# Performance work log

Hardware: AMD Instinct MI355X
Metric: run time of the kernel (lower is better)

The kernel has to match this reference:

```python
import jax, jax.numpy as jnp
import numpy as np

D, H, DH = 768, 12, 64
W = 256            # one-sided window (attention_window=512 total)
EPS = 1e-6
NEG = -1e9


def layer_norm(x, g, b):
    m = jnp.mean(x, axis=-1, keepdims=True)
    v = jnp.mean((x - m) ** 2, axis=-1, keepdims=True)
    return g * (x - m) * jax.lax.rsqrt(v + EPS) + b


def _blocks3(t, nb):
    # t: [B,H,nb,W,dh] -> keys/values of 3 neighboring blocks [B,H,nb,3W,dh]
    tp = jnp.pad(t, ((0, 0), (0, 0), (1, 1), (0, 0), (0, 0)))
    return jnp.concatenate([tp[:, :, :nb], tp[:, :, 1:nb + 1], tp[:, :, 2:nb + 2]], axis=3)


def sliding_window_attention(x, kpm, Wq, bq, Wk, bk, Wv, bv, Wo, bo):
    B, S, _ = x.shape
    nb = S // W
    def proj(Wm, bm):
        return (x @ Wm + bm).reshape(B, S, H, DH).transpose(0, 2, 1, 3).reshape(B, H, nb, W, DH)
    q = proj(Wq, bq) * (1.0 / np.sqrt(DH))
    k = proj(Wk, bk)
    v = proj(Wv, bv)
    k3 = _blocks3(k, nb)
    v3 = _blocks3(v, nb)
    # scores over local band: [B,H,nb,W,3W]
    s = jnp.einsum('bhnqd,bhnkd->bhnqk', q, k3)
    qi = jnp.arange(W)[:, None]
    kj = jnp.arange(3 * W)[None, :]
    band = jnp.abs(kj - W - qi) <= W                     # [W,3W]
    kg = (jnp.arange(nb)[:, None, None] - 1) * W + kj[None]  # global key idx [nb,1,3W]
    inrange = (kg >= 0) & (kg < S)
    # key padding mask gathered into block layout: [B,nb,3W]
    kpm_b = jnp.pad(kpm.reshape(B, nb, W), ((0, 0), (1, 1), (0, 0)), constant_values=True)
    kpm3 = jnp.concatenate([kpm_b[:, :nb], kpm_b[:, 1:nb + 1], kpm_b[:, 2:nb + 2]], axis=2)
    m = band[None, None, None] & inrange[None, None] & (~kpm3)[:, None, :, None, :]
    s = jnp.where(m, s, NEG)
    p = jax.nn.softmax(s, axis=-1)
    o = jnp.einsum('bhnqk,bhnkd->bhnqd', p, v3)
    o = o.reshape(B, H, S, DH).transpose(0, 2, 1, 3).reshape(B, S, D)
    return o @ Wo + bo


def setup_inputs() -> dict:
    key = jax.random.key(0)
    ks = jax.random.split(key, 12)
    B, S, DF = 2, 4096, 3072
    sc = 1.0 / np.sqrt(D)
    return {
        'x': jax.random.normal(ks[0], (B, S, D), jnp.float32),
        'mask': jnp.zeros((B, S), bool),
        'id': 0,
        'Wq': jax.random.normal(ks[1], (D, D), jnp.float32) * sc,
        'bq': jnp.zeros((D,), jnp.float32),
        'Wk': jax.random.normal(ks[2], (D, D), jnp.float32) * sc,
        'bk': jnp.zeros((D,), jnp.float32),
        'Wv': jax.random.normal(ks[3], (D, D), jnp.float32) * sc,
        'bv': jnp.zeros((D,), jnp.float32),
        'Wo': jax.random.normal(ks[4], (D, D), jnp.float32) * sc,
        'bo': jnp.zeros((D,), jnp.float32),
        'ln1_g': jnp.ones((D,), jnp.float32),
        'ln1_b': jnp.zeros((D,), jnp.float32),
        'W1': jax.random.normal(ks[5], (D, DF), jnp.float32) * sc,
        'b1': jnp.zeros((DF,), jnp.float32),
        'W2': jax.random.normal(ks[6], (DF, D), jnp.float32) * (1.0 / np.sqrt(DF)),
        'b2': jnp.zeros((D,), jnp.float32),
        'ln2_g': jnp.ones((D,), jnp.float32),
        'ln2_b': jnp.zeros((D,), jnp.float32),
    }


def reference(x, mask, id, Wq, bq, Wk, bk, Wv, bv, Wo, bo, ln1_g, ln1_b, W1, b1, W2, b2, ln2_g, ln2_b):
    # Sublayer 1: pre-norm residual around sliding-window self-attention
    h = layer_norm(x, ln1_g, ln1_b)
    x = x + sliding_window_attention(h, mask, Wq, bq, Wk, bk, Wv, bv, Wo, bo)
    # Sublayer 2: pre-norm residual around positionwise FFN
    h = layer_norm(x, ln2_g, ln2_b)
    x = x + (jax.nn.relu(h @ W1 + b1) @ W2 + b2)
    return x
```

## Files before the change

kernel.cpp:

```cpp
#include <hip/hip_runtime.h>
#include <hip/hip_bf16.h>
#include <cstddef>

typedef __attribute__((ext_vector_type(8))) short short8;
typedef __attribute__((ext_vector_type(4))) float f32x4;
typedef __attribute__((ext_vector_type(4))) unsigned short us4;

typedef __attribute__((address_space(1))) void as1_void;
typedef __attribute__((address_space(3))) void as3_void;

__device__ __forceinline__ void gload16(const void* g, void* lds) {
  __builtin_amdgcn_global_load_lds((as1_void*)(void*)g, (as3_void*)lds, 16, 0, 0);
}

__device__ inline unsigned short f2bf(float f) {
  union { float f; unsigned int u; } v; v.f = f;
  return (unsigned short)((v.u + 0x7FFFu + ((v.u >> 16) & 1u)) >> 16);
}

__device__ __forceinline__ float exp2v(float x) {
  float r; asm("v_exp_f32 %0, %1" : "=v"(r) : "v"(x)); return r;
}
__device__ __forceinline__ unsigned cvtpk(float a, float b) {
  unsigned r; asm("v_cvt_pk_bf16_f32 %0, %1, %2" : "=v"(r) : "v"(a), "v"(b)); return r;
}

__global__ __launch_bounds__(256) void ln_kernel(const float* __restrict__ x,
    const float* __restrict__ g, const float* __restrict__ b,
    unsigned short* __restrict__ out)
{
  int row = blockIdx.x, t = threadIdx.x;
  const float* xr = x + (size_t)row * 768;
  float v0 = xr[t], v1 = xr[t + 256], v2 = xr[t + 512];
  float s = v0 + v1 + v2;
  #pragma unroll
  for (int o = 32; o > 0; o >>= 1) s += __shfl_xor(s, o);
  __shared__ float r1[4], r2[4];
  if ((t & 63) == 0) r1[t >> 6] = s;
  __syncthreads();
  float mean = (r1[0] + r1[1] + r1[2] + r1[3]) * (1.0f / 768.0f);
  float d0 = v0 - mean, d1 = v1 - mean, d2 = v2 - mean;
  float q = d0 * d0 + d1 * d1 + d2 * d2;
  #pragma unroll
  for (int o = 32; o > 0; o >>= 1) q += __shfl_xor(q, o);
  if ((t & 63) == 0) r2[t >> 6] = q;
  __syncthreads();
  float var = (r2[0] + r2[1] + r2[2] + r2[3]) * (1.0f / 768.0f);
  float rs = rsqrtf(var + 1e-6f);
  unsigned short* orow = out + (size_t)row * 768;
  orow[t]       = f2bf(g[t]       * d0 * rs + b[t]);
  orow[t + 256] = f2bf(g[t + 256] * d1 * rs + b[t + 256]);
  orow[t + 512] = f2bf(g[t + 512] * d2 * rs + b[t + 512]);
}

__global__ __launch_bounds__(256) void prep_kernel(
    const float* __restrict__ Wq, const float* __restrict__ Wk,
    const float* __restrict__ Wv, const float* __restrict__ Wo,
    const float* __restrict__ W1, const float* __restrict__ W2,
    const float* __restrict__ bq, const float* __restrict__ bk,
    const float* __restrict__ bv,
    unsigned short* __restrict__ WTqkv, unsigned short* __restrict__ WTo,
    unsigned short* __restrict__ W1T, unsigned short* __restrict__ W2T,
    float* __restrict__ bqkv,
    const float* __restrict__ x, const float* __restrict__ ln1g,
    const float* __restrict__ ln1b, unsigned short* __restrict__ hbuf)
{
  int bid = blockIdx.x;
  int t = threadIdx.x;
  if (bid >= 6921) {
    int row = bid - 6921;
    const float* xr = x + (size_t)row * 768;
    float v0 = xr[t], v1 = xr[t + 256], v2 = xr[t + 512];
    float s = v0 + v1 + v2;
    #pragma unroll
    for (int o = 32; o > 0; o >>= 1) s += __shfl_xor(s, o);
    __shared__ float r1[4], r2[4];
    if ((t & 63) == 0) r1[t >> 6] = s;
    __syncthreads();
    float mean = (r1[0] + r1[1] + r1[2] + r1[3]) * (1.0f / 768.0f);
    float d0 = v0 - mean, d1 = v1 - mean, d2 = v2 - mean;
    float q = d0 * d0 + d1 * d1 + d2 * d2;
    #pragma unroll
    for (int o = 32; o > 0; o >>= 1) q += __shfl_xor(q, o);
    if ((t & 63) == 0) r2[t >> 6] = q;
    __syncthreads();
    float var = (r2[0] + r2[1] + r2[2] + r2[3]) * (1.0f / 768.0f);
    float rs = rsqrtf(var + 1e-6f);
    unsigned short* orow = hbuf + (size_t)row * 768;
    orow[t]       = f2bf(ln1g[t]       * d0 * rs + ln1b[t]);
    orow[t + 256] = f2bf(ln1g[t + 256] * d1 * rs + ln1b[t + 256]);
    orow[t + 512] = f2bf(ln1g[t + 512] * d2 * rs + ln1b[t + 512]);
    return;
  }
  if (bid >= 6912) {
    int i = (bid - 6912) * 256 + t;
    bqkv[i] = (i < 768) ? bq[i] : ((i < 1536) ? bk[i - 768] : bv[i - 1536]);
    return;
  }
  const float* W; unsigned short* WT; int K, N, lb;
  if (bid < 576)       { W = Wq; WT = WTqkv;                        K = 768;  N = 768;  lb = bid; }
  else if (bid < 1152) { W = Wk; WT = WTqkv + (size_t)768 * 768;    K = 768;  N = 768;  lb = bid - 576; }
  else if (bid < 1728) { W = Wv; WT = WTqkv + (size_t)1536 * 768;   K = 768;  N = 768;  lb = bid - 1152; }
  else if (bid < 2304) { W = Wo; WT = WTo;                          K = 768;  N = 768;  lb = bid - 1728; }
  else if (bid < 4608) { W = W1; WT = W1T;                          K = 768;  N = 3072; lb = bid - 2304; }
  else                 { W = W2; WT = W2T;                          K = 3072; N = 768;  lb = bid - 4608; }
  int ntN = N >> 5;
  int k0 = (lb / ntN) * 32, n0 = (lb % ntN) * 32;
  __shared__ float tile[32][33];
  int tx = t & 31, ty = t >> 5;
  #pragma unroll
  for (int i = 0; i < 32; i += 8)
    tile[ty + i][tx] = W[(size_t)(k0 + ty + i) * N + n0 + tx];
  __syncthreads();
  #pragma unroll
  for (int i = 0; i < 32; i += 8)
    WT[(size_t)(n0 + ty + i) * K + k0 + tx] = f2bf(tile[tx][ty + i]);
}

enum { EPI_QKV = 0, EPI_RELU = 1, EPI_RESID = 2 };

template<int EPI>
__global__ __launch_bounds__(256, 2) void gemmW_kernel(
    const unsigned short* __restrict__ A, const unsigned short* __restrict__ BT,
    const float* __restrict__ bias, const float* __restrict__ resid,
    void* __restrict__ outp, int M, int N, int K, int ntn)
{
  __shared__ char lds[2][40960];
  int tid = threadIdx.x;
  int nwg = gridDim.x;
  int bid = ((int)blockIdx.x & 7) * (nwg >> 3) + ((int)blockIdx.x >> 3);
  int mt = bid / ntn, nt = bid % ntn;
  int m0 = mt * 64, n0 = nt * 256;
  int w = tid >> 6, l = tid & 63;
  int fr = l & 15, fq = l >> 4;
  int rb = tid >> 3;
  int sw8 = ((tid & 7) ^ (rb & 7)) * 8;
  const unsigned short* As = A  + (size_t)(m0 + rb) * K + sw8;
  const unsigned short* Bs = BT + (size_t)(n0 + rb) * K + sw8;

  auto stage = [&](int buf, int kt) {
    char* d = &lds[buf][0] + tid * 16;
    #pragma unroll
    for (int c = 0; c < 2; c++)
      gload16(As + (size_t)(c * 32) * K + kt * 64, d + c * 4096);
    #pragma unroll
    for (int c = 0; c < 8; c++)
      gload16(Bs + (size_t)(c * 32) * K + kt * 64, d + 8192 + c * 4096);
  };

  f32x4 acc[4][4] = {};
  stage(0, 0);
  asm volatile("s_waitcnt vmcnt(0)" ::: "memory");
  __syncthreads();

  int NT = K >> 6;
  for (int t = 0; t < NT; ++t) {
    int R = t & 1;
    if (t + 1 < NT) stage(R ^ 1, t + 1);
    #pragma unroll
    for (int h = 0; h < 2; h++) {
      short8 af[4], bf[4];
      const char* base = &lds[R][0];
      int colb = (h * 64 + fq * 16) ^ ((fr & 7) << 4);
      #pragma unroll
      for (int i = 0; i < 4; i++)
        af[i] = *(const short8*)(base + (i * 16 + fr) * 128 + colb);
      #pragma unroll
      for (int j = 0; j < 4; j++)
        bf[j] = *(const short8*)(base + 8192 + (w * 64 + j * 16 + fr) * 128 + colb);
      __builtin_amdgcn_s_setprio(1);
      #pragma unroll
      for (int i = 0; i < 4; i++)
        #pragma unroll
        for (int j = 0; j < 4; j++)
          acc[i][j] = __builtin_amdgcn_mfma_f32_16x16x32_bf16(af[i], bf[j], acc[i][j], 0, 0, 0);
      __builtin_amdgcn_s_setprio(0);
    }
    asm volatile("s_waitcnt vmcnt(0)" ::: "memory");
    __syncthreads();
  }

  #pragma unroll
  for (int nj = 0; nj < 4; nj++) {
    int col = n0 + w * 64 + nj * 16 + fr;
    float bs = bias[col];
    if (EPI == EPI_QKV) {
      int which = (col >= 1536) ? 2 : ((col >= 768) ? 1 : 0);
      int c2 = col - which * 768;
      int hh = c2 >> 6, dh = c2 & 63;
      if (which == 2) {
        unsigned short* dstv = reinterpret_cast<unsigned short*>(outp) + (size_t)2 * 8192 * 768;
        #pragma unroll
        for (int i = 0; i < 4; i++) {
          int row0 = m0 + i * 16 + fq * 4;
          int bb = row0 >> 12, sl = row0 & 4095;
          us4 pv;
          #pragma unroll
          for (int r = 0; r < 4; r++) pv[r] = f2bf(acc[i][nj][r] + bs);
          *reinterpret_cast<us4*>(&dstv[((size_t)(bb * 12 + hh) * 64 + dh) * 4096 + sl]) = pv;
        }
      } else {
        unsigned short* dst = reinterpret_cast<unsigned short*>(outp) + (size_t)which * 8192 * 768;
        #pragma unroll
        for (int i = 0; i < 4; i++) {
          #pragma unroll
          for (int r = 0; r < 4; r++) {
            int row = m0 + i * 16 + fq * 4 + r;
            float c = acc[i][nj][r] + bs;
            if (which == 0) c *= 0.18033688011112042f;
            int bb = row >> 12, sl = row & 4095;
            dst[(((size_t)(bb * 12 + hh)) * 4096 + sl) * 64 + dh] = f2bf(c);
          }
        }
      }
    } else if (EPI == EPI_RELU) {
      #pragma unroll
      for (int i = 0; i < 4; i++)
        #pragma unroll
        for (int r = 0; r < 4; r++) {
          int row = m0 + i * 16 + fq * 4 + r;
          float c = fmaxf(acc[i][nj][r] + bs, 0.0f);
          reinterpret_cast<unsigned short*>(outp)[(size_t)row * N + col] = f2bf(c);
        }
    } else {
      #pragma unroll
      for (int i = 0; i < 4; i++)
        #pragma unroll
        for (int r = 0; r < 4; r++) {
          int row = m0 + i * 16 + fq * 4 + r;
          float c = acc[i][nj][r] + bs + resid[(size_t)row * N + col];
          reinterpret_cast<float*>(outp)[(size_t)row * N + col] = c;
        }
    }
  }
}

__global__ __launch_bounds__(256) void attn_fused_kernel(
    const unsigned short* __restrict__ qg, const unsigned short* __restrict__ kg,
    const unsigned short* __restrict__ vtg, const unsigned char* __restrict__ kpm,
    unsigned short* __restrict__ attn_out)
{
  __shared__ unsigned short lds_k[3][64 * 64];
  __shared__ unsigned short lds_vt[3][64 * 64];
  __shared__ unsigned short lds_p[4][32 * 64];
  int bid0 = blockIdx.x;
  int bid = (bid0 & 7) * 96 + (bid0 >> 3);
  int qblk = bid & 31, h = (bid >> 5) % 12, b = bid / 384;
  int bh = b * 12 + h;
  int q0 = qblk * 128;
  int tid = threadIdx.x, w = tid >> 6, l = tid & 63;
  int fr = l & 15, fq = l >> 4;
  int qw0 = q0 + w * 32;
  int swzb = (((l & 7) ^ (l >> 3)) << 4);
  const char* qbase  = (const char*)(qg  + (size_t)bh * 4096 * 64);
  const char* kbase  = (const char*)(kg  + (size_t)bh * 4096 * 64);
  const char* vtbase = (const char*)(vtg + (size_t)bh * 64 * 4096);
  const unsigned char* kpmb = kpm + (size_t)b * 4096;

  #pragma unroll
  for (int s = 0; s < 4; s++) {
    int row = w * 32 + s * 8 + (l >> 3);
    gload16(qbase + (size_t)(q0 + row) * 128 + swzb, (char*)lds_p[w] + s * 1024);
  }

  auto stageKVc = [&](int c, int buf) {
    int g0 = q0 - 256 + c * 64;
    g0 = (g0 < 0) ? 0 : ((g0 > 4032) ? 4032 : g0);
    #pragma unroll
    for (int s = 0; s < 2; s++) {
      int row = w * 16 + s * 8 + (l >> 3);
      gload16(kbase + (size_t)(g0 + row) * 128 + swzb,
              (char*)lds_k[buf] + (w * 2 + s) * 1024);
      gload16(vtbase + ((size_t)row * 4096 + g0) * 2 + swzb,
              (char*)lds_vt[buf] + (w * 2 + s) * 1024);
    }
  };

  stageKVc(0, 0);
  stageKVc(1, 1);
  asm volatile("s_waitcnt vmcnt(8)" ::: "memory");

  short8 qf[2][2];
  #pragma unroll
  for (int i = 0; i < 2; i++)
    #pragma unroll
    for (int ks = 0; ks < 2; ks++)
      qf[i][ks] = *(const short8*)((const char*)lds_p[w] + (i * 16 + fr) * 128 +
                    ((ks * 64 + fq * 16) ^ ((fr & 7) << 4)));

  f32x4 acc_o[2][4] = {};
  float m_st[2] = {-3.0e38f, -3.0e38f};
  float l_st[2] = {0.0f, 0.0f};

  for (int c = 0; c < 10; c++) {
    if (c < 9) { asm volatile("s_waitcnt vmcnt(4)" ::: "memory"); }
    else       { asm volatile("s_waitcnt vmcnt(0)" ::: "memory"); }
    __builtin_amdgcn_s_barrier();
    if (c < 8) stageKVc(c + 2, (c + 2) % 3);
    int g0 = q0 - 256 + c * 64;
    bool valid = (g0 >= 0) && (g0 < 4096);
    if (valid) {
      int buf = c % 3;
      unsigned int km[4];
      #pragma unroll
      for (int j = 0; j < 4; j++)
        km[j] = *(const unsigned int*)(kpmb + g0 + 16 * j + 4 * fq);
      bool anyk = __any((km[0] | km[1] | km[2] | km[3]) != 0);
      int rel = g0 - qw0;
      bool edge = anyk || (rel < -225) || (rel > 193);
      short8 kf[4][2];
      #pragma unroll
      for (int j = 0; j < 4; j++)
        #pragma unroll
        for (int ks = 0; ks < 2; ks++)
          kf[j][ks] = *(const short8*)((const char*)lds_k[buf] + (j * 16 + fr) * 128 +
                        ((ks * 64 + fq * 16) ^ ((fr & 7) << 4)));
      f32x4 accs[4][2] = {};
      #pragma unroll
      for (int j = 0; j < 4; j++)
        #pragma unroll
        for (int i = 0; i < 2; i++)
          #pragma unroll
          for (int ks = 0; ks < 2; ks++)
            accs[j][i] = __builtin_amdgcn_mfma_f32_16x16x32_bf16(kf[j][ks], qf[i][ks], accs[j][i], 0, 0, 0);
      #pragma unroll
      for (int i = 0; i < 2; i++) {
        float sv[4][4];
        #pragma unroll
        for (int j = 0; j < 4; j++)
          #pragma unroll
          for (int r = 0; r < 4; r++)
            sv[j][r] = accs[j][i][r];
        if (edge) {
          int base = rel + 4 * fq - fr - 16 * i;
          #pragma unroll
          for (int j = 0; j < 4; j++)
            #pragma unroll
            for (int r = 0; r < 4; r++) {
              int d = base + 16 * j + r;
              bool ok = (d >= -256) && (d <= 256) && (((km[j] >> (8 * r)) & 255u) == 0u);
              if (!ok) sv[j][r] = -1.0e9f;
            }
        }
        float mv = sv[0][0];
        #pragma unroll
        for (int j = 0; j < 4; j++)
          #pragma unroll
          for (int r = 0; r < 4; r++) mv = fmaxf(mv, sv[j][r]);
        mv = fmaxf(mv, __shfl_xor(mv, 16));
        mv = fmaxf(mv, __shfl_xor(mv, 32));
        float mo = m_st[i];
        if (!__all(mv - mo <= 8.0f)) {
          float mn = fmaxf(mo, mv);
          float scl = exp2v(mo - mn);
          l_st[i] *= scl;
          m_st[i] = mn;
          #pragma unroll
          for (int r = 0; r < 4; r++) {
            float so = __shfl(scl, (l & 48) | ((l >> 2) & 12) | r);
            #pragma unroll
            for (int jd = 0; jd < 4; jd++) acc_o[i][jd][r] *= so;
          }
        }
        float mn = m_st[i];
        float rs = 0.0f;
        char* prow = (char*)lds_p[w] + (i * 16 + fr) * 128;
        #pragma unroll
        for (int j = 0; j < 4; j++) {
          float p0 = exp2v(sv[j][0] - mn), p1 = exp2v(sv[j][1] - mn);
          float p2 = exp2v(sv[j][2] - mn), p3 = exp2v(sv[j][3] - mn);
          rs += (p0 + p1) + (p2 + p3);
          uint2 u; u.x = cvtpk(p0, p1); u.y = cvtpk(p2, p3);
          *(uint2*)(prow + ((32 * j + 8 * fq) ^ ((fr & 7) << 4))) = u;
        }
        rs += __shfl_xor(rs, 16);
        rs += __shfl_xor(rs, 32);
        l_st[i] += rs;
      }
      short8 pf[2][2];
      #pragma unroll
      for (int i = 0; i < 2; i++)
        #pragma unroll
        for (int ks = 0; ks < 2; ks++)
          pf[i][ks] = *(const short8*)((const char*)lds_p[w] + (i * 16 + fr) * 128 +
                        ((ks * 64 + fq * 16) ^ ((fr & 7) << 4)));
      short8 vf[4][2];
      #pragma unroll
      for (int jd = 0; jd < 4; jd++)
        #pragma unroll
        for (int ks = 0; ks < 2; ks++)
          vf[jd][ks] = *(const short8*)((const char*)lds_vt[buf] + (jd * 16 + fr) * 128 +
                        ((ks * 64 + fq * 16) ^ ((fr & 7) << 4)));
      #pragma unroll
      for (int i = 0; i < 2; i++)
        #pragma unroll
        for (int jd = 0; jd < 4; jd++)
          #pragma unroll
          for (int ks = 0; ks < 2; ks++)
            acc_o[i][jd] = __builtin_amdgcn_mfma_f32_16x16x32_bf16(pf[i][ks], vf[jd][ks], acc_o[i][jd], 0, 0, 0);
    }
  }
  #pragma unroll
  for (int i = 0; i < 2; i++) {
    #pragma unroll
    for (int r = 0; r < 4; r++) {
      float lv = __shfl(l_st[i], (l & 48) | ((l >> 2) & 12) | r);
      float inv = 1.0f / lv;
      int qrow = qw0 + i * 16 + fq * 4 + r;
      size_t orow = ((size_t)b * 4096 + qrow) * 768 + h * 64;
      #pragma unroll
      for (int jd = 0; jd < 4; jd++)
        attn_out[orow + jd * 16 + fr] = f2bf(acc_o[i][jd][r] * inv);
    }
  }
}

extern "C" void kernel_launch(void* const* d_in, const int* in_sizes, int n_in,
                              void* d_out, int out_size, void* d_ws, size_t ws_size,
                              hipStream_t stream) {
  const float* x            = (const float*)d_in[0];
  const unsigned char* mask = (const unsigned char*)d_in[1];
  const float* Wq  = (const float*)d_in[3];
  const float* bq  = (const float*)d_in[4];
  const float* Wk  = (const float*)d_in[5];
  const float* bk  = (const float*)d_in[6];
  const float* Wv  = (const float*)d_in[7];
  const float* bv  = (const float*)d_in[8];
  const float* Wo  = (const float*)d_in[9];
  const float* bo  = (const float*)d_in[10];
  const float* ln1g = (const float*)d_in[11];
  const float* ln1b = (const float*)d_in[12];
  const float* W1  = (const float*)d_in[13];
  const float* b1  = (const float*)d_in[14];
  const float* W2  = (const float*)d_in[15];
  const float* b2  = (const float*)d_in[16];
  const float* ln2g = (const float*)d_in[17];
  const float* ln2b = (const float*)d_in[18];
  float* out = (float*)d_out;

  char* ws = (char*)d_ws;
  size_t off = 0;
  auto alloc = [&](size_t bytes) -> void* {
    void* p = ws + off;
    off += (bytes + 255) & ~(size_t)255;
    return p;
  };
  unsigned short* WTqkv = (unsigned short*)alloc((size_t)2304 * 768 * 2);
  unsigned short* WTo   = (unsigned short*)alloc((size_t)768 * 768 * 2);
  unsigned short* W1T   = (unsigned short*)alloc((size_t)3072 * 768 * 2);
  unsigned short* W2T   = (unsigned short*)alloc((size_t)768 * 3072 * 2);
  float*          bqkv  = (float*)alloc(2304 * 4);
  unsigned short* hbuf  = (unsigned short*)alloc((size_t)8192 * 768 * 2);
  unsigned short* qkv   = (unsigned short*)alloc((size_t)3 * 8192 * 768 * 2);
  unsigned short* attn  = (unsigned short*)alloc((size_t)8192 * 768 * 2);
  float* x1             = (float*)alloc((size_t)8192 * 768 * 4);
  unsigned short* h2    = (unsigned short*)alloc((size_t)8192 * 768 * 2);
  unsigned short* a1    = (unsigned short*)alloc((size_t)8192 * 3072 * 2);

  prep_kernel<<<15113, 256, 0, stream>>>(Wq, Wk, Wv, Wo, W1, W2, bq, bk, bv,
                                         WTqkv, WTo, W1T, W2T, bqkv,
                                         x, ln1g, ln1b, hbuf);

  gemmW_kernel<EPI_QKV><<<1152, 256, 0, stream>>>(hbuf, WTqkv, bqkv, nullptr, qkv, 8192, 2304, 768, 9);

  attn_fused_kernel<<<768, 256, 0, stream>>>(qkv, qkv + (size_t)8192 * 768,
                                             qkv + (size_t)2 * 8192 * 768, mask, attn);

  gemmW_kernel<EPI_RESID><<<384, 256, 0, stream>>>(attn, WTo, bo, x, x1, 8192, 768, 768, 3);
  ln_kernel<<<8192, 256, 0, stream>>>(x1, ln2g, ln2b, h2);
  gemmW_kernel<EPI_RELU><<<1536, 256, 0, stream>>>(h2, W1T, b1, nullptr, a1, 8192, 3072, 768, 12);
  gemmW_kernel<EPI_RESID><<<384, 256, 0, stream>>>(a1, W2T, b2, x1, out, 8192, 768, 3072, 3);
}
```

Before: 244.1 us.

## Switch GEMMs to square 128x128 tiles with single-buffered LDS

Replaces the 64x256 double-buffered GEMM tile with a 128x128 tile over a 2x2 wave grid, using one LDS buffer per operand and no prefetch of the next K step. Square tiles cut total global traffic per output and halve LDS use, which may allow more resident workgroups per CU. In exchange, loads for each K step are no longer overlapped with the MFMA work of the previous one, so every iteration waits on memory with two barriers.

New measurement: 250.4 us. 1.03x slower.

```diff
diff --git a/kernel.cpp b/kernel.cpp
--- a/kernel.cpp
+++ b/kernel.cpp
@@ -120,54 +120,51 @@
 enum { EPI_QKV = 0, EPI_RELU = 1, EPI_RESID = 2 };
 
 template<int EPI>
-__global__ __launch_bounds__(256, 2) void gemmW_kernel(
+__global__ __launch_bounds__(256) void gemmS_kernel(
     const unsigned short* __restrict__ A, const unsigned short* __restrict__ BT,
     const float* __restrict__ bias, const float* __restrict__ resid,
     void* __restrict__ outp, int M, int N, int K, int ntn)
 {
-  __shared__ char lds[2][40960];
+  __shared__ char lds_a[16384];
+  __shared__ char lds_b[16384];
   int tid = threadIdx.x;
   int nwg = gridDim.x;
   int bid = ((int)blockIdx.x & 7) * (nwg >> 3) + ((int)blockIdx.x >> 3);
   int mt = bid / ntn, nt = bid % ntn;
-  int m0 = mt * 64, n0 = nt * 256;
+  int m0 = mt * 128, n0 = nt * 128;
   int w = tid >> 6, l = tid & 63;
+  int wr = w >> 1, wc = w & 1;
   int fr = l & 15, fq = l >> 4;
   int rb = tid >> 3;
   int sw8 = ((tid & 7) ^ (rb & 7)) * 8;
   const unsigned short* As = A  + (size_t)(m0 + rb) * K + sw8;
   const unsigned short* Bs = BT + (size_t)(n0 + rb) * K + sw8;
 
-  auto stage = [&](int buf, int kt) {
-    char* d = &lds[buf][0] + tid * 16;
-    #pragma unroll
-    for (int c = 0; c < 2; c++)
-      gload16(As + (size_t)(c * 32) * K + kt * 64, d + c * 4096);
-    #pragma unroll
-    for (int c = 0; c < 8; c++)
-      gload16(Bs + (size_t)(c * 32) * K + kt * 64, d + 8192 + c * 4096);
-  };
-
   f32x4 acc[4][4] = {};
-  stage(0, 0);
-  asm volatile("s_waitcnt vmcnt(0)" ::: "memory");
-  __syncthreads();
-
   int NT = K >> 6;
   for (int t = 0; t < NT; ++t) {
-    int R = t & 1;
-    if (t + 1 < NT) stage(R ^ 1, t + 1);
+    {
+      char* dA = lds_a + tid * 16;
+      char* dB = lds_b + tid * 16;
+      int ko = t * 64;
+      #pragma unroll
+      for (int c = 0; c < 4; c++) {
+        gload16(As + (size_t)(c * 32) * K + ko, dA + c * 4096);
+        gload16(Bs + (size_t)(c * 32) * K + ko, dB + c * 4096);
+      }
+    }
+    asm volatile("s_waitcnt vmcnt(0)" ::: "memory");
+    __syncthreads();
     #pragma unroll
     for (int h = 0; h < 2; h++) {
       short8 af[4], bf[4];
-      const char* base = &lds[R][0];
       int colb = (h * 64 + fq * 16) ^ ((fr & 7) << 4);
       #pragma unroll
       for (int i = 0; i < 4; i++)
-        af[i] = *(const short8*)(base + (i * 16 + fr) * 128 + colb);
+        af[i] = *(const short8*)(lds_a + (wr * 64 + i * 16 + fr) * 128 + colb);
       #pragma unroll
       for (int j = 0; j < 4; j++)
-        bf[j] = *(const short8*)(base + 8192 + (w * 64 + j * 16 + fr) * 128 + colb);
+        bf[j] = *(const short8*)(lds_b + (wc * 64 + j * 16 + fr) * 128 + colb);
       __builtin_amdgcn_s_setprio(1);
       #pragma unroll
       for (int i = 0; i < 4; i++)
@@ -176,13 +173,12 @@
           acc[i][j] = __builtin_amdgcn_mfma_f32_16x16x32_bf16(af[i], bf[j], acc[i][j], 0, 0, 0);
       __builtin_amdgcn_s_setprio(0);
     }
-    asm volatile("s_waitcnt vmcnt(0)" ::: "memory");
     __syncthreads();
   }
 
   #pragma unroll
   for (int nj = 0; nj < 4; nj++) {
-    int col = n0 + w * 64 + nj * 16 + fr;
+    int col = n0 + wc * 64 + nj * 16 + fr;
     float bs = bias[col];
     if (EPI == EPI_QKV) {
       int which = (col >= 1536) ? 2 : ((col >= 768) ? 1 : 0);
@@ -192,7 +188,7 @@
         unsigned short* dstv = reinterpret_cast<unsigned short*>(outp) + (size_t)2 * 8192 * 768;
         #pragma unroll
         for (int i = 0; i < 4; i++) {
-          int row0 = m0 + i * 16 + fq * 4;
+          int row0 = m0 + wr * 64 + i * 16 + fq * 4;
           int bb = row0 >> 12, sl = row0 & 4095;
           us4 pv;
           #pragma unroll
@@ -205,7 +201,7 @@
         for (int i = 0; i < 4; i++) {
           #pragma unroll
           for (int r = 0; r < 4; r++) {
-            int row = m0 + i * 16 + fq * 4 + r;
+            int row = m0 + wr * 64 + i * 16 + fq * 4 + r;
             float c = acc[i][nj][r] + bs;
             if (which == 0) c *= 0.18033688011112042f;
             int bb = row >> 12, sl = row & 4095;
@@ -218,7 +214,7 @@
       for (int i = 0; i < 4; i++)
         #pragma unroll
         for (int r = 0; r < 4; r++) {
-          int row = m0 + i * 16 + fq * 4 + r;
+          int row = m0 + wr * 64 + i * 16 + fq * 4 + r;
           float c = fmaxf(acc[i][nj][r] + bs, 0.0f);
           reinterpret_cast<unsigned short*>(outp)[(size_t)row * N + col] = f2bf(c);
         }
@@ -227,7 +223,7 @@
       for (int i = 0; i < 4; i++)
         #pragma unroll
         for (int r = 0; r < 4; r++) {
-          int row = m0 + i * 16 + fq * 4 + r;
+          int row = m0 + wr * 64 + i * 16 + fq * 4 + r;
           float c = acc[i][nj][r] + bs + resid[(size_t)row * N + col];
           reinterpret_cast<float*>(outp)[(size_t)row * N + col] = c;
         }
@@ -461,13 +457,13 @@
                                          WTqkv, WTo, W1T, W2T, bqkv,
                                          x, ln1g, ln1b, hbuf);
 
-  gemmW_kernel<EPI_QKV><<<1152, 256, 0, stream>>>(hbuf, WTqkv, bqkv, nullptr, qkv, 8192, 2304, 768, 9);
+  gemmS_kernel<EPI_QKV><<<1152, 256, 0, stream>>>(hbuf, WTqkv, bqkv, nullptr, qkv, 8192, 2304, 768, 18);
 
   attn_fused_kernel<<<768, 256, 0, stream>>>(qkv, qkv + (size_t)8192 * 768,
                                              qkv + (size_t)2 * 8192 * 768, mask, attn);
 
-  gemmW_kernel<EPI_RESID><<<384, 256, 0, stream>>>(attn, WTo, bo, x, x1, 8192, 768, 768, 3);
+  gemmS_kernel<EPI_RESID><<<384, 256, 0, stream>>>(attn, WTo, bo, x, x1, 8192, 768, 768, 6);
   ln_kernel<<<8192, 256, 0, stream>>>(x1, ln2g, ln2b, h2);
-  gemmW_kernel<EPI_RELU><<<1536, 256, 0, stream>>>(h2, W1T, b1, nullptr, a1, 8192, 3072, 768, 12);
-  gemmW_kernel<EPI_RESID><<<384, 256, 0, stream>>>(a1, W2T, b2, x1, out, 8192, 768, 3072, 3);
-}
+  gemmS_kernel<EPI_RELU><<<1536, 256, 0, stream>>>(h2, W1T, b1, nullptr, a1, 8192, 3072, 768, 24);
+  gemmS_kernel<EPI_RESID><<<384, 256, 0, stream>>>(a1, W2T, b2, x1, out, 8192, 768, 3072, 6);
+}
```
